# Performance work log

Hardware: AMD Instinct MI355X
Metric: run time of the kernel (lower is better)

## Reference

```python
import jax, jax.numpy as jnp
import numpy as np

B, T, OB = 64, 512, 256
H = 1024
AC = 8
EPS = 1e-6


def rmsnorm(x, scale):
    # RMSNorm over the last (hidden) dim with learned scale
    return x * scale * jax.lax.rsqrt(jnp.mean(x * x, axis=-1, keepdims=True) + EPS)


def lstm_layer(x, Wih, Whh, b, gnorm, cnorm):
    """RMSNorm-gated LSTM layer. x: [B,T,in] -> [B,T,H].
    Gate pre-activations are RMSNorm'd per-gate; cell state is RMSNorm'd
    before the output tanh (the norm that breaks cuDNN gate fusion)."""
    Bsz = x.shape[0]
    Hh = Whh.shape[1]
    # precompute input projection for all timesteps: [B,T,4H]
    xp = jnp.einsum('bti,gi->btg', x, Wih) + b

    def step(carry, xpt):
        h, c = carry
        z = xpt + h @ Whh.T  # [B,4H]
        zi, zf, zg, zo = jnp.split(z, 4, axis=-1)
        i = jax.nn.sigmoid(rmsnorm(zi, gnorm[0]))
        f = jax.nn.sigmoid(rmsnorm(zf, gnorm[1]))
        g = jnp.tanh(rmsnorm(zg, gnorm[2]))
        o = jax.nn.sigmoid(rmsnorm(zo, gnorm[3]))
        c = f * c + i * g
        h = o * jnp.tanh(rmsnorm(c, cnorm))
        return (h, c), h

    init = (jnp.zeros((Bsz, Hh), x.dtype), jnp.zeros((Bsz, Hh), x.dtype))
    _, hs = jax.lax.scan(step, init, jnp.swapaxes(xp, 0, 1))  # [T,B,H]
    return jnp.swapaxes(hs, 0, 1)


def setup_inputs() -> dict:
    key = jax.random.key(0)
    ks = jax.random.split(key, 12)

    def w(k, shape, fan_in):
        return jax.random.normal(k, shape, dtype=jnp.float32) / np.sqrt(fan_in)

    return {
        'obs': jax.random.normal(ks[0], (B, T, OB), dtype=jnp.float32),
        'Wih0': w(ks[1], (4 * H, OB), OB),
        'Whh0': w(ks[2], (4 * H, H), H),
        'b0': jnp.zeros((4 * H,), jnp.float32),
        'gnorm0': jnp.ones((4, H), jnp.float32),
        'cnorm0': jnp.ones((H,), jnp.float32),
        'Wih1': w(ks[3], (4 * H, H), H),
        'Whh1': w(ks[4], (4 * H, H), H),
        'b1': jnp.zeros((4 * H,), jnp.float32),
        'gnorm1': jnp.ones((4, H), jnp.float32),
        'cnorm1': jnp.ones((H,), jnp.float32),
        'Wout': w(ks[5], (AC, H), H),
        'bout': jnp.zeros((AC,), jnp.float32),
        'std_param': jnp.zeros((AC,), jnp.float32),
    }


def reference(obs, Wih0, Whh0, b0, gnorm0, cnorm0,
              Wih1, Whh1, b1, gnorm1, cnorm1,
              Wout, bout, std_param):
    out = lstm_layer(obs, Wih0, Whh0, b0, gnorm0, cnorm0)
    out = lstm_layer(out, Wih1, Whh1, b1, gnorm1, cnorm1)
    features = out[:, -1, :]              # last timestep, like out[:, -1, :]
    mean = features @ Wout.T + bout       # [B, AC]
    std = jax.nn.softplus(std_param) + 0.01  # global learned std, [AC]
    return mean, std
```

## Files before the change

kernel.cpp:

```cpp
#include <hip/hip_runtime.h>
#include <hip/hip_bf16.h>

typedef __attribute__((ext_vector_type(8))) __bf16 bf16x8;
typedef __attribute__((ext_vector_type(4))) float f32x4;
typedef unsigned short u16;
typedef unsigned int u32;
typedef unsigned long long u64;

#define NB 64
#define NT 512
#define NH 1024
#define NOB 256
#define NWG 256
#define HALF_WG 128
#define G4H 4096
#define BH (NB*NH)

#define S_OBS 0
#define S_H0  16384
#define S_H1  81920
#define LDS_TOTAL 147456

#define KT0 10
#define KT1 16

#define AS_RELAXED __ATOMIC_RELAXED
#define SCOPE_AGENT __HIP_MEMORY_SCOPE_AGENT
#define KEEPW(x) asm volatile("" : "+v"(x))

#define SBAR  do { asm volatile("s_barrier" ::: "memory"); __builtin_amdgcn_sched_barrier(0); } while (0)
#define LGKM0 do { asm volatile("s_waitcnt lgkmcnt(0)" ::: "memory"); __builtin_amdgcn_sched_barrier(0); } while (0)
#define VMW0  do { asm volatile("s_waitcnt vmcnt(0)" ::: "memory"); __builtin_amdgcn_sched_barrier(0); } while (0)
#define VMW8  do { asm volatile("s_waitcnt vmcnt(8)" ::: "memory"); __builtin_amdgcn_sched_barrier(0); } while (0)

__device__ __forceinline__ u16 f2bf(float f) {
  __hip_bfloat16 h = __float2bfloat16(f);
  return *reinterpret_cast<u16*>(&h);
}
__device__ __forceinline__ float sigm(float x) { return 1.f / (1.f + __expf(-x)); }
__device__ __forceinline__ float tanh_f(float x) {
  float e = __expf(2.f * x);
  return 1.f - 2.f / (e + 1.f);
}

__device__ __forceinline__ void gload_lds16(const void* g, void* l) {
  __builtin_amdgcn_global_load_lds(
      (const __attribute__((address_space(1))) void*)g,
      (__attribute__((address_space(3))) void*)l, 16, 0, 0);
}

__device__ __forceinline__ int4 load_b128_coh(const void* p) {
  int4 v;
  asm volatile("global_load_dwordx4 %0, %1, off sc0 sc1\n\ts_waitcnt vmcnt(0)"
               : "=v"(v) : "v"(p) : "memory");
  return v;
}
__device__ __forceinline__ u64 AL64(const u64* p) {
  return __hip_atomic_load(p, AS_RELAXED, SCOPE_AGENT);
}

__device__ __forceinline__ void gridbar(int* barD, int myleaf, int gen) {
  __syncthreads();
  if (threadIdx.x < 64) {
    const int lane = threadIdx.x;
    if (lane == 0)
      __hip_atomic_fetch_add(&barD[myleaf * 32], 1, AS_RELAXED, SCOPE_AGENT);
    const int tgt = HALF_WG * gen;
    for (;;) {
      int v = (lane < 16)
            ? __hip_atomic_load(&barD[lane * 32], AS_RELAXED, SCOPE_AGENT) : 0;
#pragma unroll
      for (int off = 8; off; off >>= 1) v += __shfl_xor(v, off);
      v = __shfl(v, 0);
      if (v >= tgt) break;
      __builtin_amdgcn_s_sleep(1);
    }
  }
  __syncthreads();
}

__device__ __host__ __forceinline__ int wavek0(int kq, int kt) {
  return kt < 2 ? kq * 64 + kt * 32 : 256 + kq * 256 + (kt - 2) * 32;
}
__device__ __host__ __forceinline__ int wavek1(int kq, int kt) {
  return kq * 512 + kt * 32;
}

template<int LAYER>
__global__ void __launch_bounds__(256)
pack_weights(const float* __restrict__ Wih, const float* __restrict__ Whh,
             u16* __restrict__ wp) {
  constexpr int KT = LAYER ? KT1 : KT0;
  constexpr int KIN = LAYER ? 1024 : 256;
  const int total = 128 * 2 * 4 * KT * 64;
  for (int idx = blockIdx.x * blockDim.x + threadIdx.x; idx < total;
       idx += gridDim.x * blockDim.x) {
    int lane = idx & 63;
    int q = idx >> 6;
    int kt = q % KT; q /= KT;
    int kq = q & 3; q >>= 2;
    int nt = q & 1; q >>= 1;
    int slice = q;
    int outr = slice * 32 + nt * 16 + (lane & 15);
    int kb = (LAYER ? wavek1(kq, kt) : wavek0(kq, kt)) + (lane >> 4) * 8;
    union { u16 uu[8]; int4 qv; } vv;
#pragma unroll
    for (int j = 0; j < 8; ++j) {
      int k = kb + j;
      float f = (k < KIN) ? Wih[(long)outr * KIN + k] : Whh[(long)outr * NH + (k - KIN)];
      vv.uu[j] = f2bf(f);
    }
    reinterpret_cast<int4*>(wp)[idx] = vv.qv;
  }
}

__global__ void __launch_bounds__(256)
transpose_obs(const float* __restrict__ obs, u16* __restrict__ obsT) {
  long idx = (long)blockIdx.x * blockDim.x + threadIdx.x;
  if (idx >= (long)NT * NB * NOB) return;
  int k = (int)(idx & (NOB - 1));
  long r = idx >> 8;
  int b = (int)(r & (NB - 1));
  int t = (int)(r >> 6);
  obsT[idx] = f2bf(obs[((long)b * NT + t) * NOB + k]);
}

template<bool H1COH>
__global__ void __launch_bounds__(512)
fused_lstm(const u16* __restrict__ obsT,
           const u16* __restrict__ wp0, const u16* __restrict__ wp1,
           const float* __restrict__ b0, const float* __restrict__ gn0,
           const float* __restrict__ cn0,
           const float* __restrict__ b1, const float* __restrict__ gn1,
           const float* __restrict__ cn1,
           u16* __restrict__ h0hist, u16* __restrict__ h1buf, long long h1step,
           float* __restrict__ zbuf, float* __restrict__ feat,
           int* __restrict__ bar) {
  extern __shared__ char smem[];
  f32x4* sred = reinterpret_cast<f32x4*>(smem + S_H1);
  float* p2red = reinterpret_cast<float*>(smem + S_H0);

  const int tid = threadIdx.x;
  const int lane = tid & 63;
  const int wave = tid >> 6;
  const int nt = wave & 1;
  const int kq = wave >> 1;
  const int col = lane & 15;
  const int rgrp = lane >> 4;
  const int wg = blockIdx.x;
  const int bg = wg >> 7;
  const int slice = wg & 127;
  const int kl = (wave & 1) * 64 + lane;
  const int w2 = wave >> 1;
  int* barD = bar + bg * 512;
  const int myleaf = slice & 15;

  bf16x8 wf0[KT0], wf1[KT1];
  {
    const bf16x8* p0 = reinterpret_cast<const bf16x8*>(wp0)
                     + ((size_t)((slice * 2 + nt) * 4 + kq) * KT0) * 64 + lane;
#pragma unroll
    for (int u = 0; u < KT0; ++u) { wf0[u] = p0[u * 64]; KEEPW(wf0[u]); }
    const bf16x8* p1 = reinterpret_cast<const bf16x8*>(wp1)
                     + ((size_t)((slice * 2 + nt) * 4 + kq) * KT1) * 64 + lane;
#pragma unroll
    for (int u = 0; u < KT1; ++u) { wf1[u] = p1[u * 64]; KEEPW(wf1[u]); }
  }

  const bool p2wg = (slice < 64);
  const int l2 = (slice >> 5) & 1;
  const int prow = bg * 32 + (slice & 31);
  const int ej = tid * 2;
  float gn[8];
  float cw0 = 0.f, cw1 = 0.f;
  float c0 = 0.f, c1 = 0.f;
  if (p2wg) {
    const float* gnp = l2 ? gn1 : gn0;
    const float* cnp = l2 ? cn1 : cn0;
#pragma unroll
    for (int g = 0; g < 4; ++g) {
      gn[g * 2]     = gnp[g * NH + ej];
      gn[g * 2 + 1] = gnp[g * NH + ej + 1];
    }
    cw0 = cnp[ej];
    cw1 = cnp[ej + 1];
  }
  constexpr float inv = 1.f / 1024.f;

  {
    const u16* os = obsT + (size_t)(bg * 32) * NOB;
#pragma unroll
    for (int i = 0; i < 2; ++i) {
      const int row = 16 * i + 2 * wave + (lane >> 5);
      gload_lds16(os + (size_t)row * NOB + (size_t)(((lane & 31) ^ (row & 7)) * 8),
                  smem + S_OBS + (i * 512 + wave * 64) * 16);
    }
  }

  int gen = 0;

  for (int r = 0; r <= NT; ++r) {
    const u16* h0s = h0hist + (size_t)r * BH + (size_t)(bg * 32) * NH;
    const u16* h1s = h1buf + (size_t)r * h1step + (size_t)(bg * 32) * NH;
#pragma unroll
    for (int i = 0; i < 8; ++i) {
      const int row = i * 4 + w2;
      const int koff = (kl ^ (row & 7)) * 8;
      gload_lds16(h0s + (size_t)row * NH + koff,
                  smem + S_H0 + (i * 512 + wave * 64) * 16);
    }
    if constexpr (!H1COH) {
#pragma unroll
      for (int i = 0; i < 8; ++i) {
        const int row = i * 4 + w2;
        const int koff = (kl ^ (row & 7)) * 8;
        gload_lds16(h1s + (size_t)row * NH + koff,
                    smem + S_H1 + (i * 512 + wave * 64) * 16);
      }
      VMW8;
      SBAR;
    } else {
#pragma unroll 1
      for (int c = tid; c < 4096; c += 512) {
        int row = c >> 7, kc = c & 127;
        int4 v = load_b128_coh(h1s + (size_t)row * NH + kc * 8);
        *reinterpret_cast<int4*>(smem + S_H1 + row * 2048 + ((kc ^ (row & 7)) << 4)) = v;
      }
      VMW0; LGKM0;
      SBAR;
    }

    f32x4 a00 = {0,0,0,0}, a01 = {0,0,0,0};
    f32x4 a10 = {0,0,0,0}, a11 = {0,0,0,0};
    if (r < NT) {
#pragma unroll
      for (int kt = 0; kt < KT0; ++kt) {
        const int base   = (kt < 2) ? S_OBS : S_H0;
        const int rowstr = (kt < 2) ? 512 : 2048;
        const int chunk0 = (kt < 2) ? (kq * 8 + kt * 4) : (kq * 32 + (kt - 2) * 4);
        const int sw = (((chunk0 + rgrp) ^ (col & 7)) << 4);
        bf16x8 am0 = *reinterpret_cast<const bf16x8*>(smem + base + col * rowstr + sw);
        bf16x8 am1 = *reinterpret_cast<const bf16x8*>(smem + base + (16 + col) * rowstr + sw);
        a00 = __builtin_amdgcn_mfma_f32_16x16x32_bf16(am0, wf0[kt], a00, 0, 0, 0);
        a01 = __builtin_amdgcn_mfma_f32_16x16x32_bf16(am1, wf0[kt], a01, 0, 0, 0);
      }
    }
    if constexpr (!H1COH) {
      VMW0;
      SBAR;
    }

    if (r >= 1) {
      const int base = (kq < 2) ? S_H0 : S_H1;
#pragma unroll
      for (int kt = 0; kt < KT1; ++kt) {
        const int chunk0 = (kq & 1) * 64 + kt * 4;
        const int sw = (((chunk0 + rgrp) ^ (col & 7)) << 4);
        bf16x8 am0 = *reinterpret_cast<const bf16x8*>(smem + base + col * 2048 + sw);
        bf16x8 am1 = *reinterpret_cast<const bf16x8*>(smem + base + (16 + col) * 2048 + sw);
        a10 = __builtin_amdgcn_mfma_f32_16x16x32_bf16(am0, wf1[kt], a10, 0, 0, 0);
        a11 = __builtin_amdgcn_mfma_f32_16x16x32_bf16(am1, wf1[kt], a11, 0, 0, 0);
      }
    }
    LGKM0;
    SBAR;

    {
      f32x4* pw = sred + wave * 512 + lane;
      pw[0 * 64] = a00;
      pw[1 * 64] = a01;
      pw[2 * 64] = a10;
      pw[3 * 64] = a11;
    }
    LGKM0;
    SBAR;
    {
      const int q = tid >> 6, ln = tid & 63;
      const int fcol = ln & 15, frg = ln >> 4;
      const int lm = q & 3;
      const int nq2 = q >> 2;
      f32x4 s = sred[(nq2 + 0) * 512 + lm * 64 + ln]
              + sred[(nq2 + 2) * 512 + lm * 64 + ln]
              + sred[(nq2 + 4) * 512 + lm * 64 + ln]
              + sred[(nq2 + 6) * 512 + lm * 64 + ln];
      const int l = lm >> 1, m = lm & 1;
      const bool zv = l ? (r >= 1) : (r < NT);
      if (zv) {
        const int outg = slice * 32 + nq2 * 16 + fcol;
        const float bv = (l ? b1 : b0)[outg];
        float* zr = zbuf + ((size_t)l * NB + bg * 32 + m * 16 + frg * 4) * G4H + outg;
#pragma unroll
        for (int j = 0; j < 4; ++j)
          __hip_atomic_store(&zr[(size_t)j * G4H], s[j] + bv, AS_RELAXED, SCOPE_AGENT);
      }
    }
    gridbar(barD, myleaf, ++gen);

    if (r + 1 < NT) {
      const u16* os = obsT + (size_t)(r + 1) * (NB * NOB) + (size_t)(bg * 32) * NOB;
#pragma unroll
      for (int i = 0; i < 2; ++i) {
        const int row = 16 * i + 2 * wave + (lane >> 5);
        gload_lds16(os + (size_t)row * NOB + (size_t)(((lane & 31) ^ (row & 7)) * 8),
                    smem + S_OBS + (i * 512 + wave * 64) * 16);
      }
    }

    if (p2wg && (l2 ? (r >= 1) : (r < NT))) {
      const u64* zq = reinterpret_cast<const u64*>(
          zbuf + ((size_t)l2 * NB + prow) * G4H);
      union { u64 q; float f[2]; } va, vb, vg, vo;
      va.q = AL64(zq + tid);
      vb.q = AL64(zq + 512 + tid);
      vg.q = AL64(zq + 1024 + tid);
      vo.q = AL64(zq + 1536 + tid);
      float s0 = va.f[0] * va.f[0] + va.f[1] * va.f[1];
      float s1 = vb.f[0] * vb.f[0] + vb.f[1] * vb.f[1];
      float s2 = vg.f[0] * vg.f[0] + vg.f[1] * vg.f[1];
      float s3 = vo.f[0] * vo.f[0] + vo.f[1] * vo.f[1];
#pragma unroll
      for (int off = 32; off; off >>= 1) {
        s0 += __shfl_xor(s0, off);
        s1 += __shfl_xor(s1, off);
        s2 += __shfl_xor(s2, off);
        s3 += __shfl_xor(s3, off);
      }
      if (lane == 0) {
        float* sp = p2red + wave * 4;
        sp[0] = s0; sp[1] = s1; sp[2] = s2; sp[3] = s3;
      }
      __syncthreads();
      float t0 = 0.f, t1 = 0.f, t2 = 0.f, t3 = 0.f;
#pragma unroll
      for (int w = 0; w < 8; ++w) {
        t0 += p2red[w * 4 + 0]; t1 += p2red[w * 4 + 1];
        t2 += p2red[w * 4 + 2]; t3 += p2red[w * 4 + 3];
      }
      const float r0 = rsqrtf(t0 * inv + 1e-6f);
      const float r1 = rsqrtf(t1 * inv + 1e-6f);
      const float r2 = rsqrtf(t2 * inv + 1e-6f);
      const float r3 = rsqrtf(t3 * inv + 1e-6f);
      const float i0 = sigm(va.f[0] * gn[0] * r0), i1 = sigm(va.f[1] * gn[1] * r0);
      const float f0 = sigm(vb.f[0] * gn[2] * r1), f1 = sigm(vb.f[1] * gn[3] * r1);
      const float g0 = tanh_f(vg.f[0] * gn[4] * r2), g1 = tanh_f(vg.f[1] * gn[5] * r2);
      const float o0 = sigm(vo.f[0] * gn[6] * r3), o1 = sigm(vo.f[1] * gn[7] * r3);
      c0 = f0 * c0 + i0 * g0;
      c1 = f1 * c1 + i1 * g1;
      float cs = c0 * c0 + c1 * c1;
#pragma unroll
      for (int off = 32; off; off >>= 1) cs += __shfl_xor(cs, off);
      if (lane == 0) p2red[32 + wave] = cs;
      __syncthreads();
      float ct = 0.f;
#pragma unroll
      for (int w = 0; w < 8; ++w) ct += p2red[32 + w];
      const float rc = rsqrtf(ct * inv + 1e-6f);
      const float hx = o0 * tanh_f(c0 * cw0 * rc);
      const float hy = o1 * tanh_f(c1 * cw1 * rc);
      u16* hw;
      if (l2 == 0) hw = h0hist + (size_t)(r + 1) * BH + (size_t)prow * NH + ej;
      else         hw = h1buf + (size_t)(r + 1) * h1step + (size_t)prow * NH + ej;
      const u32 packed = (u32)f2bf(hx) | ((u32)f2bf(hy) << 16);
      __hip_atomic_store(reinterpret_cast<u32*>(hw), packed, AS_RELAXED, SCOPE_AGENT);
      if (l2 == 1 && r == NT) {
        feat[(size_t)prow * NH + ej] = hx;
        feat[(size_t)prow * NH + ej + 1] = hy;
      }
    }
    gridbar(barD, myleaf, ++gen);
  }
}

__global__ void __launch_bounds__(256)
head_kernel(const float* __restrict__ feat, const float* __restrict__ Wout,
            const float* __restrict__ bout, const float* __restrict__ stdp,
            float* __restrict__ out) {
  int b = blockIdx.x;
  int a = threadIdx.x >> 5;
  int l = threadIdx.x & 31;
  float s = 0.f;
  for (int k = l; k < NH; k += 32) s += feat[b * NH + k] * Wout[a * NH + k];
#pragma unroll
  for (int off = 16; off; off >>= 1) s += __shfl_xor(s, off, 32);
  if (l == 0) out[b * 8 + a] = s + bout[a];
  if (b == 0 && threadIdx.x < 8) {
    float x = stdp[threadIdx.x];
    float splus = (x > 20.f) ? x : log1pf(__expf(x));
    out[512 + threadIdx.x] = splus + 0.01f;
  }
}

extern "C" void kernel_launch(void* const* d_in, const int* in_sizes, int n_in,
                              void* d_out, int out_size, void* d_ws, size_t ws_size,
                              hipStream_t stream) {
  (void)in_sizes; (void)n_in; (void)out_size;
  const float* obs  = (const float*)d_in[0];
  const float* Wih0 = (const float*)d_in[1];
  const float* Whh0 = (const float*)d_in[2];
  const float* b0   = (const float*)d_in[3];
  const float* gn0  = (const float*)d_in[4];
  const float* cn0  = (const float*)d_in[5];
  const float* Wih1 = (const float*)d_in[6];
  const float* Whh1 = (const float*)d_in[7];
  const float* b1   = (const float*)d_in[8];
  const float* gn1  = (const float*)d_in[9];
  const float* cn1  = (const float*)d_in[10];
  const float* Wout = (const float*)d_in[11];
  const float* bout = (const float*)d_in[12];
  const float* stdp = (const float*)d_in[13];
  float* out = (float*)d_out;

  char* ws = (char*)d_ws;
  size_t off = 0;
  auto take = [&](size_t bytes) -> char* {
    char* p = ws + off;
    off = (off + bytes + 255) & ~(size_t)255;
    return p;
  };

  const size_t WP0_B  = (size_t)128 * 2 * 4 * KT0 * 64 * 16;
  const size_t WP1_B  = (size_t)128 * 2 * 4 * KT1 * 64 * 16;
  const size_t OBST_B = (size_t)NT * NB * NOB * 2;
  const size_t H0H_B  = (size_t)(NT + 1) * BH * 2;
  const size_t H1H_B  = (size_t)(NT + 2) * BH * 2;

  u16* wp0    = (u16*)take(WP0_B);
  u16* wp1    = (u16*)take(WP1_B);
  u16* obsT   = (u16*)take(OBST_B);
  u16* h0hist = (u16*)take(H0H_B);
  u16* h1b    = (u16*)take(H1H_B);
  float* zbuf = (float*)take((size_t)2 * NB * G4H * 4);
  float* feat = (float*)take((size_t)NB * NH * 4);
  int* bars   = (int*)take(8192);
  bool fits = (off <= ws_size);
  long long h1step = BH;

  if (!fits) {
    off = 0;
    wp0    = (u16*)take(WP0_B);
    wp1    = (u16*)take(WP1_B);
    obsT   = (u16*)take(OBST_B);
    h0hist = (u16*)take(H0H_B);
    h1b    = (u16*)take((size_t)BH * 2);
    zbuf   = (float*)take((size_t)2 * NB * G4H * 4);
    feat   = (float*)take((size_t)NB * NH * 4);
    bars   = (int*)take(8192);
    h1step = 0;
    if (off > ws_size) return;
  }

  (void)hipFuncSetAttribute((const void*)fused_lstm<false>,
                            hipFuncAttributeMaxDynamicSharedMemorySize, LDS_TOTAL);
  (void)hipFuncSetAttribute((const void*)fused_lstm<true>,
                            hipFuncAttributeMaxDynamicSharedMemorySize, LDS_TOTAL);

  (void)hipMemsetAsync(bars, 0, 8192, stream);
  (void)hipMemsetAsync(h0hist, 0, (size_t)BH * 2, stream);
  (void)hipMemsetAsync(h1b, 0, (size_t)(fits ? 2 : 1) * BH * 2, stream);

  pack_weights<0><<<2560, 256, 0, stream>>>(Wih0, Whh0, wp0);
  pack_weights<1><<<4096, 256, 0, stream>>>(Wih1, Whh1, wp1);
  transpose_obs<<<(NT * NB * NOB) / 256, 256, 0, stream>>>(obs, obsT);

  if (fits) {
    fused_lstm<false><<<NWG, 512, LDS_TOTAL, stream>>>(
        obsT, wp0, wp1, b0, gn0, cn0, b1, gn1, cn1,
        h0hist, h1b, h1step, zbuf, feat, bars);
  } else {
    fused_lstm<true><<<NWG, 512, LDS_TOTAL, stream>>>(
        obsT, wp0, wp1, b0, gn0, cn0, b1, gn1, cn1,
        h0hist, h1b, 0LL, zbuf, feat, bars);
  }

  head_kernel<<<NB, 256, 0, stream>>>(feat, Wout, bout, stdp, out);
}
```

Measured before the change: 5.209 ms.

## Replace full grid barrier with per-gate-group counters polled before z loads

The full grid barrier after the z-buffer stores is replaced by a per-group arrive counter. Slices are now grouped by slice>>3, so each counter covers eight workgroups. The gate-activation workgroups spin on only the counters covering the gate slices they read, one gate chunk at a time, and load each chunk as soon as it is ready. This is meant to cut the wait for stragglers and let obs prefetch and early loads overlap. It assumes each counter group maps exactly to one gate chunk's producers, and polling with s_sleep adds latency and memory traffic.

```diff
diff --git a/kernel.cpp b/kernel.cpp
--- a/kernel.cpp
+++ b/kernel.cpp
@@ -153,7 +153,7 @@
   const int kl = (wave & 1) * 64 + lane;
   const int w2 = wave >> 1;
   int* barD = bar + bg * 512;
-  const int myleaf = slice & 15;
+  const int myleaf = slice >> 3;
 
   bf16x8 wf0[KT0], wf1[KT1];
   {
@@ -294,7 +294,11 @@
           __hip_atomic_store(&zr[(size_t)j * G4H], s[j] + bv, AS_RELAXED, SCOPE_AGENT);
       }
     }
-    gridbar(barD, myleaf, ++gen);
+
+    const int bar1gen = ++gen;
+    __syncthreads();
+    if (tid == 0)
+      __hip_atomic_fetch_add(&barD[myleaf * 32], 1, AS_RELAXED, SCOPE_AGENT);
 
     if (r + 1 < NT) {
       const u16* os = obsT + (size_t)(r + 1) * (NB * NOB) + (size_t)(bg * 32) * NOB;
@@ -309,25 +313,30 @@
     if (p2wg && (l2 ? (r >= 1) : (r < NT))) {
       const u64* zq = reinterpret_cast<const u64*>(
           zbuf + ((size_t)l2 * NB + prow) * G4H);
-      union { u64 q; float f[2]; } va, vb, vg, vo;
-      va.q = AL64(zq + tid);
-      vb.q = AL64(zq + 512 + tid);
-      vg.q = AL64(zq + 1024 + tid);
-      vo.q = AL64(zq + 1536 + tid);
-      float s0 = va.f[0] * va.f[0] + va.f[1] * va.f[1];
-      float s1 = vb.f[0] * vb.f[0] + vb.f[1] * vb.f[1];
-      float s2 = vg.f[0] * vg.f[0] + vg.f[1] * vg.f[1];
-      float s3 = vo.f[0] * vo.f[0] + vo.f[1] * vo.f[1];
+      const int k2 = wave >> 1;
+      union UZ { u64 q; float f[2]; } vz[4];
+      float ss[4];
+#pragma unroll
+      for (int g = 0; g < 4; ++g) {
+        if (lane == 0) {
+          while (__hip_atomic_load(&barD[(4 * g + k2) * 32], AS_RELAXED, SCOPE_AGENT)
+                 < 8 * bar1gen)
+            __builtin_amdgcn_s_sleep(1);
+        }
+        __builtin_amdgcn_sched_barrier(0);
+        vz[g].q = AL64(zq + g * 512 + tid);
+        ss[g] = vz[g].f[0] * vz[g].f[0] + vz[g].f[1] * vz[g].f[1];
+      }
 #pragma unroll
       for (int off = 32; off; off >>= 1) {
-        s0 += __shfl_xor(s0, off);
-        s1 += __shfl_xor(s1, off);
-        s2 += __shfl_xor(s2, off);
-        s3 += __shfl_xor(s3, off);
+        ss[0] += __shfl_xor(ss[0], off);
+        ss[1] += __shfl_xor(ss[1], off);
+        ss[2] += __shfl_xor(ss[2], off);
+        ss[3] += __shfl_xor(ss[3], off);
       }
       if (lane == 0) {
         float* sp = p2red + wave * 4;
-        sp[0] = s0; sp[1] = s1; sp[2] = s2; sp[3] = s3;
+        sp[0] = ss[0]; sp[1] = ss[1]; sp[2] = ss[2]; sp[3] = ss[3];
       }
       __syncthreads();
       float t0 = 0.f, t1 = 0.f, t2 = 0.f, t3 = 0.f;
@@ -340,10 +349,10 @@
       const float r1 = rsqrtf(t1 * inv + 1e-6f);
       const float r2 = rsqrtf(t2 * inv + 1e-6f);
       const float r3 = rsqrtf(t3 * inv + 1e-6f);
-      const float i0 = sigm(va.f[0] * gn[0] * r0), i1 = sigm(va.f[1] * gn[1] * r0);
-      const float f0 = sigm(vb.f[0] * gn[2] * r1), f1 = sigm(vb.f[1] * gn[3] * r1);
-      const float g0 = tanh_f(vg.f[0] * gn[4] * r2), g1 = tanh_f(vg.f[1] * gn[5] * r2);
-      const float o0 = sigm(vo.f[0] * gn[6] * r3), o1 = sigm(vo.f[1] * gn[7] * r3);
+      const float i0 = sigm(vz[0].f[0] * gn[0] * r0), i1 = sigm(vz[0].f[1] * gn[1] * r0);
+      const float f0 = sigm(vz[1].f[0] * gn[2] * r1), f1 = sigm(vz[1].f[1] * gn[3] * r1);
+      const float g0 = tanh_f(vz[2].f[0] * gn[4] * r2), g1 = tanh_f(vz[2].f[1] * gn[5] * r2);
+      const float o0 = sigm(vz[3].f[0] * gn[6] * r3), o1 = sigm(vz[3].f[1] * gn[7] * r3);
       c0 = f0 * c0 + i0 * g0;
       c1 = f1 * c1 + i1 * g1;
       float cs = c0 * c0 + c1 * c1;
```

After: 5.888 ms. 13.0% more time.
